# Kernel tuning notes

Hardware: AMD Instinct MI355X
Metric: run time of the kernel (lower is better)

## Reference

```python
import jax, jax.numpy as jnp
import numpy as np

B, G = 256, 24
N = B * G
D_IN, HEADS, D_HEAD = 128, 8, 64  # out_channels = in_channels//2 = 64, concat=False
EFF = HEADS * D_HEAD
EPS = 1e-5
SCALE = float(np.sqrt(D_HEAD))

def _gelu(x):
    return jax.nn.gelu(x, approximate=False)

def _pff(x, w1, b1, w2, b2):
    # PositionwiseFeedForward, dropout=0 (eval)
    return _gelu(x @ w1.T + b1) @ w2.T + b2

def _graph_norm_global(x, w, b, ms):
    # GraphNorm called without batch -> single graph over all N nodes
    mean = jnp.mean(x, axis=0, keepdims=True)
    out = x - mean * ms
    var = jnp.mean(out * out, axis=0, keepdims=True)
    return w * out / jnp.sqrt(var + EPS) + b

def _graph_norm(x, w, b, ms, batch, nseg):
    cnt = jax.ops.segment_sum(jnp.ones((x.shape[0],), x.dtype), batch, nseg)[:, None]
    mean = jax.ops.segment_sum(x, batch, nseg) / cnt
    out = x - mean[batch] * ms
    var = jax.ops.segment_sum(out * out, batch, nseg) / cnt
    return w * out / jnp.sqrt(var + EPS)[batch] + b

def _segment_softmax(logits, seg, nseg):
    m = jax.ops.segment_max(logits, seg, num_segments=nseg)
    e = jnp.exp(logits - m[seg])
    s = jax.ops.segment_sum(e, seg, num_segments=nseg)
    return e / (s[seg] + 1e-16)

def _attn_conv(x, edge_index, p):
    (nq_w, nq_b, nq_ms, wq, bq, wk, bk, wv, bv,
     no_w, no_b, no_ms, o_w1, o_b1, o_w2, o_b2) = p
    n = x.shape[0]
    xin = x
    xn = _graph_norm_global(x, nq_w, nq_b, nq_ms)
    q = (xn @ wq.T + bq).reshape(n, HEADS, D_HEAD)
    k = (xn @ wk.T + bk).reshape(n, HEADS, D_HEAD)
    v = (xn @ wv.T + bv).reshape(n, HEADS, D_HEAD)
    loops = jnp.arange(n, dtype=edge_index.dtype)  # add_self_loops appends
    src = jnp.concatenate([edge_index[0], loops])
    dst = jnp.concatenate([edge_index[1], loops])
    qk = jnp.sum(q[dst] * k[src], axis=-1) / SCALE          # [E', H]
    alpha = _segment_softmax(qk, dst, n)                     # segment softmax over dst
    aggr = jax.ops.segment_sum(v[src] * alpha[:, :, None], dst, num_segments=n)  # [N,H,Dh]
    aggr = aggr.mean(axis=1)                                 # concat=False: head mean -> [N,64]
    init = xin.reshape(n, D_IN // D_HEAD, D_HEAD).sum(axis=1)  # sum-fold 128 -> 64 residual
    h = aggr + init
    hn = _graph_norm_global(h, no_w, no_b, no_ms)
    return h + _pff(hn, o_w1, o_b1, o_w2, o_b2)


def setup_inputs() -> dict:
    key = jax.random.key(0)
    ks = jax.random.split(key, 12)
    # block-dense edges: fully connected within each set, no self loops
    a = np.arange(G)
    ii, jj = np.meshgrid(a, a, indexing='ij')
    m = ii != jj
    dst_l, src_l = ii[m], jj[m]
    offs = (np.arange(B) * G)[:, None]
    src = (src_l[None, :] + offs).reshape(-1)
    dst = (dst_l[None, :] + offs).reshape(-1)
    edge_index = jnp.asarray(np.stack([src, dst]), dtype=jnp.int64)
    batch = jnp.asarray(np.repeat(np.arange(B), G), dtype=jnp.int64)
    ptr = jnp.asarray(np.arange(B + 1) * G, dtype=jnp.int64)
    x = jax.random.normal(ks[0], (N, D_IN), jnp.float32)
    def lin(k, o, i):
        return jax.random.normal(k, (o, i), jnp.float32) * (1.0 / np.sqrt(i))
    d = dict(x=x, edge_index=edge_index, ptr=ptr, batch=batch)
    d.update(nq_w=jnp.ones((D_IN,)), nq_b=jnp.zeros((D_IN,)), nq_ms=jnp.ones((D_IN,)))
    d.update(wq=lin(ks[1], EFF, D_IN), bq=jnp.zeros((EFF,)),
             wk=lin(ks[2], EFF, D_IN), bk=jnp.zeros((EFF,)),
             wv=lin(ks[3], EFF, D_IN), bv=jnp.zeros((EFF,)))
    d.update(no_w=jnp.ones((D_HEAD,)), no_b=jnp.zeros((D_HEAD,)), no_ms=jnp.ones((D_HEAD,)))
    d.update(o_w1=lin(ks[4], D_HEAD, D_HEAD), o_b1=jnp.zeros((D_HEAD,)),
             o_w2=lin(ks[5], D_HEAD, D_HEAD), o_b2=jnp.zeros((D_HEAD,)))
    d.update(pn_w=jnp.ones((D_HEAD,)), pn_b=jnp.zeros((D_HEAD,)), pn_ms=jnp.ones((D_HEAD,)))
    d.update(p_w1=lin(ks[6], D_HEAD, D_HEAD), p_b1=jnp.zeros((D_HEAD,)),
             p_w2=lin(ks[7], 1, D_HEAD), p_b2=jnp.zeros((1,)))
    return d


def reference(x, edge_index, ptr, batch,
              nq_w, nq_b, nq_ms, wq, bq, wk, bk, wv, bv,
              no_w, no_b, no_ms, o_w1, o_b1, o_w2, o_b2,
              pn_w, pn_b, pn_ms, p_w1, p_b1, p_w2, p_b2):
    nseg = ptr.shape[0] - 1
    h = _attn_conv(x, edge_index,
                   (nq_w, nq_b, nq_ms, wq, bq, wk, bk, wv, bv,
                    no_w, no_b, no_ms, o_w1, o_b1, o_w2, o_b2))   # [N,64]
    hn = _graph_norm(h, pn_w, pn_b, pn_ms, batch, nseg)
    score = _pff(hn, p_w1, p_b1, p_w2, p_b2)                       # [N,1]
    w = _segment_softmax(score[:, 0], batch, nseg)[:, None]        # per-set softmax
    return jax.ops.segment_sum(x * w, batch, num_segments=nseg)    # [B, 128]
```

## Files before the change

kernel.cpp:

```cpp
#include <hip/hip_runtime.h>
#include <stdint.h>


#define N_NODES 6144
#define GSIZE 24
#define NGRAPH 256
#define DIN 128
#define DH 64
#define EFF 512
#define EPSN 1e-5f

typedef __attribute__((ext_vector_type(8))) __bf16 bf16x8;
typedef __attribute__((ext_vector_type(4))) float f32x4;
union U16B { uint4 u; bf16x8 v; unsigned short s[8]; };

__device__ inline unsigned short f2bf(float f){
  unsigned u = __float_as_uint(f);
  u += 0x7fff + ((u>>16)&1);
  return (unsigned short)(u>>16);
}
__device__ inline float gelu_exact(float x){ return 0.5f*x*(1.0f+erff(x*0.70710678118654752f)); }

#define XP    0
#define HP    49152
#define WT1   81920
#define WT2   86016
#define PWT1  90112
#define FBo   94208
#define WCVT_BYTE  385024
#define HCOMB_BYTE 778240

#define QSTRIDE 516

__global__ __launch_bounds__(256)
void k_pre(const float* __restrict__ x,
           const float* __restrict__ o_w1, const float* __restrict__ o_w2,
           const float* __restrict__ p_w1,
           const float* __restrict__ o_b1, const float* __restrict__ o_b2,
           const float* __restrict__ p_b1, const float* __restrict__ p_w2,
           const float* __restrict__ p_b2,
           const float* __restrict__ wq, const float* __restrict__ wk,
           const float* __restrict__ wv,
           float* __restrict__ wsf){
  int t = threadIdx.x;
  int bi = blockIdx.x;
  if(bi < 192){
    int c = t & 127, h = t >> 7;
    float s = 0.f, q = 0.f;
    #pragma unroll
    for(int r = 0; r < 16; ++r){
      float v = x[(size_t)(bi*32 + h + 2*r)*DIN + c];
      s += v; q += v*v;
    }
    __shared__ float sm[256], sm2[256];
    sm[t] = s; sm2[t] = q;
    __syncthreads();
    if(t < 128){
      wsf[XP + bi*256 + t]       = sm[t] + sm[t+128];
      wsf[XP + bi*256 + 128 + t] = sm2[t] + sm2[t+128];
    }
    return;
  }
  if(bi < 195){
    const float* src; float* dst;
    if(bi == 192){ src = o_w1; dst = wsf + WT1; }
    else if(bi == 193){ src = o_w2; dst = wsf + WT2; }
    else { src = p_w1; dst = wsf + PWT1; }
    for(int p = t; p < DH*DH; p += 256){
      int r = p >> 6, c = p & 63;
      dst[c*DH + r] = src[p];
    }
    if(bi == 192){
      float* fb = wsf + FBo;
      if(t < 64){
        fb[t]       = o_b1[t];
        fb[64 + t]  = o_b2[t];
        fb[128 + t] = p_b1[t];
        fb[192 + t] = p_w2[t];
      }
      if(t == 0) fb[256] = p_b2[0];
    }
    return;
  }
  int j = bi - 195;
  int mat = j >> 2, seg = j & 3;
  const float* src = (mat==0) ? wq : (mat==1) ? wk : wv;
  unsigned short* dst = (unsigned short*)((char*)wsf + WCVT_BYTE)
                        + (size_t)mat*EFF*DIN + seg*16384;
  const float* sp = src + seg*16384;
  for(int e = t*8; e < 16384; e += 2048){
    float4 a = *(const float4*)(sp + e);
    float4 b = *(const float4*)(sp + e + 4);
    U16B o;
    o.s[0]=f2bf(a.x); o.s[1]=f2bf(a.y); o.s[2]=f2bf(a.z); o.s[3]=f2bf(a.w);
    o.s[4]=f2bf(b.x); o.s[5]=f2bf(b.y); o.s[6]=f2bf(b.z); o.s[7]=f2bf(b.w);
    *(uint4*)(dst + e) = o.u;
  }
}

__global__ __launch_bounds__(512)
void k_attn2(const float* __restrict__ x,
             const float* __restrict__ bq, const float* __restrict__ bk,
             const float* __restrict__ bv,
             const float* __restrict__ nq_w, const float* __restrict__ nq_b,
             const float* __restrict__ nq_ms,
             float* __restrict__ ws, float* __restrict__ hcomb){
  __shared__ __align__(16) float qlds[3*GSIZE*QSTRIDE];
  __shared__ __align__(16) float hv[GSIZE][68];
  __shared__ float A1s[DIN], C1s[DIN];

  int t = threadIdx.x, g = blockIdx.x, base = g*GSIZE;
  int h = t >> 6, l = t & 63;
  const unsigned short* wcvt = (const unsigned short*)((const char*)ws + WCVT_BYTE);

  for(int i = t; i < GSIZE*68; i += 512) ((float*)hv)[i] = 0.f;

  {
    float* redA = qlds;
    float* redB = qlds + 512;
    int c = t & 127, grp = t >> 7;
    float s = 0.f, q = 0.f;
    for(int p = grp*48; p < grp*48 + 48; ++p){
      s += ws[XP + p*256 + c];
      q += ws[XP + p*256 + 128 + c];
    }
    redA[t] = s; redB[t] = q;
    __syncthreads();
    if(t < 128){
      float s1 = redA[t] + redA[t+128] + redA[t+256] + redA[t+384];
      float q1 = redB[t] + redB[t+128] + redB[t+256] + redB[t+384];
      float mean = s1 * (1.0f / N_NODES);
      float ex2  = q1 * (1.0f / N_NODES);
      float cm   = mean * nq_ms[t];
      float var  = ex2 - 2.f*cm*mean + cm*cm;
      float rstd = rsqrtf(var + EPSN);
      float a    = nq_w[t] * rstd;
      A1s[t] = a; C1s[t] = nq_b[t] - a*cm;
    }
    __syncthreads();
  }

  int m = l & 15, lq = l >> 4;

  bf16x8 afr[2][4];
  #pragma unroll
  for(int mt = 0; mt < 2; ++mt){
    int row = mt*16 + m; if(row > GSIZE-1) row = GSIZE-1;
    const float* xr = x + (size_t)(base + row)*DIN;
    #pragma unroll
    for(int kk = 0; kk < 4; ++kk){
      int k0 = kk*32 + lq*8;
      float4 a = *(const float4*)(xr + k0);
      float4 b = *(const float4*)(xr + k0 + 4);
      U16B u;
      u.s[0] = f2bf(a.x*A1s[k0+0] + C1s[k0+0]);
      u.s[1] = f2bf(a.y*A1s[k0+1] + C1s[k0+1]);
      u.s[2] = f2bf(a.z*A1s[k0+2] + C1s[k0+2]);
      u.s[3] = f2bf(a.w*A1s[k0+3] + C1s[k0+3]);
      u.s[4] = f2bf(b.x*A1s[k0+4] + C1s[k0+4]);
      u.s[5] = f2bf(b.y*A1s[k0+5] + C1s[k0+5]);
      u.s[6] = f2bf(b.z*A1s[k0+6] + C1s[k0+6]);
      u.s[7] = f2bf(b.w*A1s[k0+7] + C1s[k0+7]);
      afr[mt][kk] = u.v;
    }
  }

  #pragma unroll
  for(int nt = 0; nt < 12; ++nt){
    int mat = nt >> 2, sub = nt & 3;
    const unsigned short* wp = wcvt + (size_t)mat*EFF*DIN
                             + (size_t)(h*64 + sub*16 + m)*DIN + lq*8;
    const float* bias = (mat==0) ? bq : (mat==1) ? bk : bv;
    float4 bb = *(const float4*)(bias + h*64 + sub*16 + lq*4);
    f32x4 acc0 = {0.f,0.f,0.f,0.f}, acc1 = {0.f,0.f,0.f,0.f};
    #pragma unroll
    for(int kk = 0; kk < 4; ++kk){
      U16B w8; w8.u = *(const uint4*)(wp + kk*32);
      acc0 = __builtin_amdgcn_mfma_f32_16x16x32_bf16(w8.v, afr[0][kk], acc0, 0, 0, 0);
      acc1 = __builtin_amdgcn_mfma_f32_16x16x32_bf16(w8.v, afr[1][kk], acc1, 0, 0, 0);
    }
    float* dst = qlds + mat*(GSIZE*QSTRIDE);
    int col = h*64 + sub*16 + lq*4;
    {
      float4 o; o.x = acc0[0]+bb.x; o.y = acc0[1]+bb.y; o.z = acc0[2]+bb.z; o.w = acc0[3]+bb.w;
      *(float4*)(dst + m*QSTRIDE + col) = o;
    }
    if(m < 8){
      float4 o; o.x = acc1[0]+bb.x; o.y = acc1[1]+bb.y; o.z = acc1[2]+bb.z; o.w = acc1[3]+bb.w;
      *(float4*)(dst + (16+m)*QSTRIDE + col) = o;
    }
  }

  {
    int r0 = 3*(l >> 3), j0 = 3*(l & 7);
    const float* qp = qlds + r0*QSTRIDE + h*64;
    const float* kp = qlds + GSIZE*QSTRIDE + j0*QSTRIDE + h*64;
    float s00=0.f,s01=0.f,s02=0.f,s10=0.f,s11=0.f,s12=0.f,s20=0.f,s21=0.f,s22=0.f;
    #pragma unroll
    for(int d4 = 0; d4 < 16; ++d4){
      float4 q0 = *(const float4*)(qp + d4*4);
      float4 q1 = *(const float4*)(qp + QSTRIDE + d4*4);
      float4 q2 = *(const float4*)(qp + 2*QSTRIDE + d4*4);
      float4 k0 = *(const float4*)(kp + d4*4);
      float4 k1 = *(const float4*)(kp + QSTRIDE + d4*4);
      float4 k2 = *(const float4*)(kp + 2*QSTRIDE + d4*4);
      s00 += q0.x*k0.x + q0.y*k0.y + q0.z*k0.z + q0.w*k0.w;
      s01 += q0.x*k1.x + q0.y*k1.y + q0.z*k1.z + q0.w*k1.w;
      s02 += q0.x*k2.x + q0.y*k2.y + q0.z*k2.z + q0.w*k2.w;
      s10 += q1.x*k0.x + q1.y*k0.y + q1.z*k0.z + q1.w*k0.w;
      s11 += q1.x*k1.x + q1.y*k1.y + q1.z*k1.z + q1.w*k1.w;
      s12 += q1.x*k2.x + q1.y*k2.y + q1.z*k2.z + q1.w*k2.w;
      s20 += q2.x*k0.x + q2.y*k0.y + q2.z*k0.z + q2.w*k0.w;
      s21 += q2.x*k1.x + q2.y*k1.y + q2.z*k1.z + q2.w*k1.w;
      s22 += q2.x*k2.x + q2.y*k2.y + q2.z*k2.z + q2.w*k2.w;
    }
    float a0, a1, a2, m0, su, inv;
    float* STb = qlds + h*64;
    a0 = s00*0.125f; a1 = s01*0.125f; a2 = s02*0.125f;
    m0 = fmaxf(fmaxf(a0, a1), a2);
    #pragma unroll
    for(int o = 1; o < 8; o <<= 1) m0 = fmaxf(m0, __shfl_xor(m0, o, 8));
    a0 = __expf(a0-m0); a1 = __expf(a1-m0); a2 = __expf(a2-m0);
    su = a0 + a1 + a2;
    #pragma unroll
    for(int o = 1; o < 8; o <<= 1) su += __shfl_xor(su, o, 8);
    inv = 1.0f/(su + 1e-16f);
    STb[(j0+0)*QSTRIDE + r0] = a0*inv; STb[(j0+1)*QSTRIDE + r0] = a1*inv; STb[(j0+2)*QSTRIDE + r0] = a2*inv;
    a0 = s10*0.125f; a1 = s11*0.125f; a2 = s12*0.125f;
    m0 = fmaxf(fmaxf(a0, a1), a2);
    #pragma unroll
    for(int o = 1; o < 8; o <<= 1) m0 = fmaxf(m0, __shfl_xor(m0, o, 8));
    a0 = __expf(a0-m0); a1 = __expf(a1-m0); a2 = __expf(a2-m0);
    su = a0 + a1 + a2;
    #pragma unroll
    for(int o = 1; o < 8; o <<= 1) su += __shfl_xor(su, o, 8);
    inv = 1.0f/(su + 1e-16f);
    STb[(j0+0)*QSTRIDE + r0+1] = a0*inv; STb[(j0+1)*QSTRIDE + r0+1] = a1*inv; STb[(j0+2)*QSTRIDE + r0+1] = a2*inv;
    a0 = s20*0.125f; a1 = s21*0.125f; a2 = s22*0.125f;
    m0 = fmaxf(fmaxf(a0, a1), a2);
    #pragma unroll
    for(int o = 1; o < 8; o <<= 1) m0 = fmaxf(m0, __shfl_xor(m0, o, 8));
    a0 = __expf(a0-m0); a1 = __expf(a1-m0); a2 = __expf(a2-m0);
    su = a0 + a1 + a2;
    #pragma unroll
    for(int o = 1; o < 8; o <<= 1) su += __shfl_xor(su, o, 8);
    inv = 1.0f/(su + 1e-16f);
    STb[(j0+0)*QSTRIDE + r0+2] = a0*inv; STb[(j0+1)*QSTRIDE + r0+2] = a1*inv; STb[(j0+2)*QSTRIDE + r0+2] = a2*inv;
  }

  {
    float o24[GSIZE];
    #pragma unroll
    for(int r = 0; r < GSIZE; ++r) o24[r] = 0.f;
    const float* vp  = qlds + 2*GSIZE*QSTRIDE + h*64 + l;
    const float* STb = qlds + h*64;
    #pragma unroll
    for(int j = 0; j < GSIZE; ++j){
      float v = vp[j*QSTRIDE];
      #pragma unroll
      for(int rq = 0; rq < 6; ++rq){
        float4 p4 = *(const float4*)(STb + j*QSTRIDE + rq*4);
        o24[rq*4+0] = fmaf(p4.x, v, o24[rq*4+0]);
        o24[rq*4+1] = fmaf(p4.y, v, o24[rq*4+1]);
        o24[rq*4+2] = fmaf(p4.z, v, o24[rq*4+2]);
        o24[rq*4+3] = fmaf(p4.w, v, o24[rq*4+3]);
      }
    }
    #pragma unroll
    for(int r = 0; r < GSIZE; ++r) atomicAdd(&hv[r][l], o24[r]);
  }
  __syncthreads();

  #pragma unroll
  for(int sl = 0; sl < 3; ++sl){
    int idx = t + sl*512;
    int r = idx >> 6, d = idx & 63;
    const float* xr = x + (size_t)(base + r)*DIN;
    float hval = hv[r][d]*0.125f + xr[d] + xr[64 + d];
    hcomb[(size_t)(base + r)*DH + d] = hval;
    hv[r][d] = hval;
  }
  __syncthreads();
  if(t < 64){
    float s1 = 0.f, s2 = 0.f;
    #pragma unroll
    for(int i = 0; i < GSIZE; ++i){ float v = hv[i][t]; s1 += v; s2 += v*v; }
    ws[HP + g*128 + t]      = s1;
    ws[HP + g*128 + 64 + t] = s2;
  }
}

__global__ __launch_bounds__(256)
void k_final(const float* __restrict__ x,
             const float* __restrict__ hbuf, const float* __restrict__ ws,
             const float* __restrict__ no_w, const float* __restrict__ no_b,
             const float* __restrict__ no_ms,
             const float* __restrict__ pn_w, const float* __restrict__ pn_b,
             const float* __restrict__ pn_ms,
             float* __restrict__ out){
  __shared__ __align__(16) float W1[4096];
  __shared__ __align__(16) float W2[4096];
  __shared__ __align__(16) float PW1[4096];
  __shared__ __align__(16) float fbs[260];
  __shared__ __align__(16) float hs[GSIZE][68];
  __shared__ __align__(16) float hn[GSIZE][68];
  __shared__ __align__(16) float ts[GSIZE][68];
  __shared__ float A2s[DH], C2s[DH];
  __shared__ float a3[DH], c3[DH];
  __shared__ float scores[GSIZE], wsm[GSIZE];
  __shared__ float redA[256], redB[256];

  int t = threadIdx.x;
  int base = blockIdx.x * GSIZE;
  int c = t & 63, i0 = t >> 6;

  {
    const float4* s1 = (const float4*)(ws + WT1);
    const float4* s2 = (const float4*)(ws + WT2);
    const float4* s3 = (const float4*)(ws + PWT1);
    #pragma unroll
    for(int it = 0; it < 4; ++it){
      int i = t + it*256;
      ((float4*)W1)[i]  = s1[i];
      ((float4*)W2)[i]  = s2[i];
      ((float4*)PW1)[i] = s3[i];
    }
    if(t < 257) fbs[t] = ws[FBo + t];
    int cc = t & 63, grp = t >> 6;
    float s1r = 0.f, s2r = 0.f;
    for(int p = grp; p < NGRAPH; p += 4){
      s1r += ws[HP + p*128 + cc];
      s2r += ws[HP + p*128 + 64 + cc];
    }
    redA[t] = s1r; redB[t] = s2r;
  }
  __syncthreads();
  if(t < DH){
    float a1 = redA[t] + redA[t+64] + redA[t+128] + redA[t+192];
    float a2 = redB[t] + redB[t+64] + redB[t+128] + redB[t+192];
    float mean = a1 * (1.0f / N_NODES);
    float ex2  = a2 * (1.0f / N_NODES);
    float cm   = mean * no_ms[t];
    float var  = ex2 - 2.f*cm*mean + cm*cm;
    float rstd = rsqrtf(var + EPSN);
    float a    = no_w[t] * rstd;
    A2s[t] = a; C2s[t] = no_b[t] - a*cm;
  }
  __syncthreads();
  {
    float a2 = A2s[c];
    float c2 = C2s[c];
    #pragma unroll
    for(int r = 0; r < 6; ++r){
      int i = i0 + 4*r;
      float hvv = hbuf[(size_t)(base + i)*DH + c];
      hs[i][c] = hvv;
      hn[i][c] = a2*hvv + c2;
    }
  }
  __syncthreads();

  {
    float acc[6];
    #pragma unroll
    for(int r = 0; r < 6; ++r) acc[r] = fbs[c];
    #pragma unroll 16
    for(int k = 0; k < DH; ++k){
      float w = W1[k*DH + c];
      #pragma unroll
      for(int r = 0; r < 6; ++r) acc[r] = fmaf(hn[i0 + 4*r][k], w, acc[r]);
    }
    #pragma unroll
    for(int r = 0; r < 6; ++r) ts[i0 + 4*r][c] = gelu_exact(acc[r]);
  }
  __syncthreads();

  {
    float acc[6];
    #pragma unroll
    for(int r = 0; r < 6; ++r) acc[r] = fbs[64 + c];
    #pragma unroll 16
    for(int k = 0; k < DH; ++k){
      float w = W2[k*DH + c];
      #pragma unroll
      for(int r = 0; r < 6; ++r) acc[r] = fmaf(ts[i0 + 4*r][k], w, acc[r]);
    }
    #pragma unroll
    for(int r = 0; r < 6; ++r) hs[i0 + 4*r][c] += acc[r];
  }
  __syncthreads();

  if(t < DH){
    float s1 = 0.f, s2 = 0.f;
    #pragma unroll
    for(int i = 0; i < GSIZE; i++){ float v = hs[i][t]; s1 += v; s2 += v*v; }
    float mean = s1 * (1.0f / GSIZE);
    float ex2  = s2 * (1.0f / GSIZE);
    float cm   = mean * pn_ms[t];
    float var  = ex2 - 2.f*cm*mean + cm*cm;
    float rstd = rsqrtf(var + EPSN);
    float a    = pn_w[t] * rstd;
    a3[t] = a; c3[t] = pn_b[t] - a*cm;
  }
  __syncthreads();

  {
    float acc[6];
    #pragma unroll
    for(int r = 0; r < 6; ++r) acc[r] = fbs[128 + c];
    #pragma unroll 16
    for(int k = 0; k < DH; ++k){
      float w  = PW1[k*DH + c];
      float ak = a3[k], ck = c3[k];
      #pragma unroll
      for(int r = 0; r < 6; ++r){
        float hnv = fmaf(ak, hs[i0 + 4*r][k], ck);
        acc[r] = fmaf(hnv, w, acc[r]);
      }
    }
    #pragma unroll
    for(int r = 0; r < 6; ++r) ts[i0 + 4*r][c] = gelu_exact(acc[r]);
  }
  __syncthreads();

  if(t < GSIZE){
    const float4* tp = (const float4*)ts[t];
    const float4* wp = (const float4*)(fbs + 192);
    float s = fbs[256];
    #pragma unroll
    for(int q = 0; q < 16; ++q){
      float4 a = tp[q], b = wp[q];
      s += a.x*b.x + a.y*b.y + a.z*b.z + a.w*b.w;
    }
    scores[t] = s;
  }
  __syncthreads();
  if(t < GSIZE){
    float mx = -1e30f;
    #pragma unroll
    for(int j = 0; j < GSIZE; j++) mx = fmaxf(mx, scores[j]);
    float sum = 0.f;
    #pragma unroll
    for(int j = 0; j < GSIZE; j++) sum += __expf(scores[j] - mx);
    wsm[t] = __expf(scores[t] - mx) / (sum + 1e-16f);
  }
  __syncthreads();
  if(t < DIN){
    float s = 0.f;
    #pragma unroll 8
    for(int i = 0; i < GSIZE; i++) s += wsm[i] * x[(size_t)(base+i)*DIN + t];
    out[(size_t)blockIdx.x*DIN + t] = s;
  }
}

extern "C" void kernel_launch(void* const* d_in, const int* in_sizes, int n_in,
                              void* d_out, int out_size, void* d_ws, size_t ws_size,
                              hipStream_t stream){
  (void)in_sizes; (void)n_in; (void)out_size; (void)ws_size;
  const float* x    = (const float*)d_in[0];
  const float* nq_w = (const float*)d_in[4];
  const float* nq_b = (const float*)d_in[5];
  const float* nq_ms= (const float*)d_in[6];
  const float* wq   = (const float*)d_in[7];
  const float* bq   = (const float*)d_in[8];
  const float* wk   = (const float*)d_in[9];
  const float* bk   = (const float*)d_in[10];
  const float* wv   = (const float*)d_in[11];
  const float* bv   = (const float*)d_in[12];
  const float* no_w = (const float*)d_in[13];
  const float* no_b = (const float*)d_in[14];
  const float* no_ms= (const float*)d_in[15];
  const float* o_w1 = (const float*)d_in[16];
  const float* o_b1 = (const float*)d_in[17];
  const float* o_w2 = (const float*)d_in[18];
  const float* o_b2 = (const float*)d_in[19];
  const float* pn_w = (const float*)d_in[20];
  const float* pn_b = (const float*)d_in[21];
  const float* pn_ms= (const float*)d_in[22];
  const float* p_w1 = (const float*)d_in[23];
  const float* p_b1 = (const float*)d_in[24];
  const float* p_w2 = (const float*)d_in[25];
  const float* p_b2 = (const float*)d_in[26];

  float* ws    = (float*)d_ws;
  float* hcomb = (float*)((char*)d_ws + HCOMB_BYTE);

  k_pre<<<207, 256, 0, stream>>>(x, o_w1, o_w2, p_w1, o_b1, o_b2, p_b1, p_w2, p_b2,
                                 wq, wk, wv, ws);
  k_attn2<<<NGRAPH, 512, 0, stream>>>(x, bq, bk, bv, nq_w, nq_b, nq_ms, ws, hcomb);
  k_final<<<NGRAPH, 256, 0, stream>>>(x, hcomb, ws, no_w, no_b, no_ms,
                                      pn_w, pn_b, pn_ms, (float*)d_out);
}
```

Baseline: 181.0 us.

## Reduce global norm statistics with atomics and software-pipeline QKV weight loads

The per-block column sums and sums of squares for both global GraphNorms are now accumulated with atomicAdd into small buffers that are zeroed by a memset. Each consumer block reads one finished value instead of re-reducing 192 or 256 partials, which removes redundant reduction work in every block of k_attn2 and k_final. The QKV MFMA loop is also unrolled by hand with triple-buffered weight registers so global loads overlap the MFMAs. The costs are an extra memset launch, atomic contention, nondeterministic float summation order, and higher register pressure.

```diff
diff --git a/kernel.cpp b/kernel.cpp
--- a/kernel.cpp
+++ b/kernel.cpp
@@ -21,8 +21,8 @@
 }
 __device__ inline float gelu_exact(float x){ return 0.5f*x*(1.0f+erff(x*0.70710678118654752f)); }
 
-#define XP    0
-#define HP    49152
+#define XS    0
+#define HS    256
 #define WT1   81920
 #define WT2   86016
 #define PWT1  90112
@@ -56,8 +56,8 @@
     sm[t] = s; sm2[t] = q;
     __syncthreads();
     if(t < 128){
-      wsf[XP + bi*256 + t]       = sm[t] + sm[t+128];
-      wsf[XP + bi*256 + 128 + t] = sm2[t] + sm2[t+128];
+      atomicAdd(&wsf[XS + t],       sm[t] + sm[t+128]);
+      atomicAdd(&wsf[XS + 128 + t], sm2[t] + sm2[t+128]);
     }
     return;
   }
@@ -98,6 +98,40 @@
   }
 }
 
+#define LOADW(nt, W, B) do{ \
+  const int mat_ = (nt)>>2, sub_ = (nt)&3; \
+  const unsigned short* wp_ = wcvt + (size_t)mat_*EFF*DIN \
+      + (size_t)(h*64 + sub_*16 + m)*DIN + lq*8; \
+  W[0] = *(const uint4*)(wp_);      W[1] = *(const uint4*)(wp_ + 32); \
+  W[2] = *(const uint4*)(wp_ + 64); W[3] = *(const uint4*)(wp_ + 96); \
+  const float* bias_ = (mat_==0) ? bq : (mat_==1) ? bk : bv; \
+  B = *(const float4*)(bias_ + h*64 + sub_*16 + lq*4); \
+}while(0)
+
+#define COMPW(nt, W, B) do{ \
+  const int mat_ = (nt)>>2, sub_ = (nt)&3; \
+  f32x4 a0_ = {0.f,0.f,0.f,0.f}, a1_ = {0.f,0.f,0.f,0.f}; \
+  U16B w8_; \
+  w8_.u = W[0]; \
+  a0_ = __builtin_amdgcn_mfma_f32_16x16x32_bf16(w8_.v, afr[0][0], a0_, 0, 0, 0); \
+  a1_ = __builtin_amdgcn_mfma_f32_16x16x32_bf16(w8_.v, afr[1][0], a1_, 0, 0, 0); \
+  w8_.u = W[1]; \
+  a0_ = __builtin_amdgcn_mfma_f32_16x16x32_bf16(w8_.v, afr[0][1], a0_, 0, 0, 0); \
+  a1_ = __builtin_amdgcn_mfma_f32_16x16x32_bf16(w8_.v, afr[1][1], a1_, 0, 0, 0); \
+  w8_.u = W[2]; \
+  a0_ = __builtin_amdgcn_mfma_f32_16x16x32_bf16(w8_.v, afr[0][2], a0_, 0, 0, 0); \
+  a1_ = __builtin_amdgcn_mfma_f32_16x16x32_bf16(w8_.v, afr[1][2], a1_, 0, 0, 0); \
+  w8_.u = W[3]; \
+  a0_ = __builtin_amdgcn_mfma_f32_16x16x32_bf16(w8_.v, afr[0][3], a0_, 0, 0, 0); \
+  a1_ = __builtin_amdgcn_mfma_f32_16x16x32_bf16(w8_.v, afr[1][3], a1_, 0, 0, 0); \
+  float* dst_ = qlds + mat_*(GSIZE*QSTRIDE); \
+  const int col_ = h*64 + sub_*16 + lq*4; \
+  { float4 o_; o_.x=a0_[0]+B.x; o_.y=a0_[1]+B.y; o_.z=a0_[2]+B.z; o_.w=a0_[3]+B.w; \
+    *(float4*)(dst_ + m*QSTRIDE + col_) = o_; } \
+  if(m < 8){ float4 o_; o_.x=a1_[0]+B.x; o_.y=a1_[1]+B.y; o_.z=a1_[2]+B.z; o_.w=a1_[3]+B.w; \
+    *(float4*)(dst_ + (16+m)*QSTRIDE + col_) = o_; } \
+}while(0)
+
 __global__ __launch_bounds__(512)
 void k_attn2(const float* __restrict__ x,
              const float* __restrict__ bq, const float* __restrict__ bk,
@@ -115,30 +149,18 @@
 
   for(int i = t; i < GSIZE*68; i += 512) ((float*)hv)[i] = 0.f;
 
-  {
-    float* redA = qlds;
-    float* redB = qlds + 512;
-    int c = t & 127, grp = t >> 7;
-    float s = 0.f, q = 0.f;
-    for(int p = grp*48; p < grp*48 + 48; ++p){
-      s += ws[XP + p*256 + c];
-      q += ws[XP + p*256 + 128 + c];
-    }
-    redA[t] = s; redB[t] = q;
-    __syncthreads();
-    if(t < 128){
-      float s1 = redA[t] + redA[t+128] + redA[t+256] + redA[t+384];
-      float q1 = redB[t] + redB[t+128] + redB[t+256] + redB[t+384];
-      float mean = s1 * (1.0f / N_NODES);
-      float ex2  = q1 * (1.0f / N_NODES);
-      float cm   = mean * nq_ms[t];
-      float var  = ex2 - 2.f*cm*mean + cm*cm;
-      float rstd = rsqrtf(var + EPSN);
-      float a    = nq_w[t] * rstd;
-      A1s[t] = a; C1s[t] = nq_b[t] - a*cm;
-    }
-    __syncthreads();
-  }
+  if(t < 128){
+    float s1 = ws[XS + t];
+    float q1 = ws[XS + 128 + t];
+    float mean = s1 * (1.0f / N_NODES);
+    float ex2  = q1 * (1.0f / N_NODES);
+    float cm   = mean * nq_ms[t];
+    float var  = ex2 - 2.f*cm*mean + cm*cm;
+    float rstd = rsqrtf(var + EPSN);
+    float a    = nq_w[t] * rstd;
+    A1s[t] = a; C1s[t] = nq_b[t] - a*cm;
+  }
+  __syncthreads();
 
   int m = l & 15, lq = l >> 4;
 
@@ -165,30 +187,22 @@
     }
   }
 
-  #pragma unroll
-  for(int nt = 0; nt < 12; ++nt){
-    int mat = nt >> 2, sub = nt & 3;
-    const unsigned short* wp = wcvt + (size_t)mat*EFF*DIN
-                             + (size_t)(h*64 + sub*16 + m)*DIN + lq*8;
-    const float* bias = (mat==0) ? bq : (mat==1) ? bk : bv;
-    float4 bb = *(const float4*)(bias + h*64 + sub*16 + lq*4);
-    f32x4 acc0 = {0.f,0.f,0.f,0.f}, acc1 = {0.f,0.f,0.f,0.f};
-    #pragma unroll
-    for(int kk = 0; kk < 4; ++kk){
-      U16B w8; w8.u = *(const uint4*)(wp + kk*32);
-      acc0 = __builtin_amdgcn_mfma_f32_16x16x32_bf16(w8.v, afr[0][kk], acc0, 0, 0, 0);
-      acc1 = __builtin_amdgcn_mfma_f32_16x16x32_bf16(w8.v, afr[1][kk], acc1, 0, 0, 0);
-    }
-    float* dst = qlds + mat*(GSIZE*QSTRIDE);
-    int col = h*64 + sub*16 + lq*4;
-    {
-      float4 o; o.x = acc0[0]+bb.x; o.y = acc0[1]+bb.y; o.z = acc0[2]+bb.z; o.w = acc0[3]+bb.w;
-      *(float4*)(dst + m*QSTRIDE + col) = o;
-    }
-    if(m < 8){
-      float4 o; o.x = acc1[0]+bb.x; o.y = acc1[1]+bb.y; o.z = acc1[2]+bb.z; o.w = acc1[3]+bb.w;
-      *(float4*)(dst + (16+m)*QSTRIDE + col) = o;
-    }
+  {
+    uint4 wA[4], wB[4], wC[4];
+    float4 bA, bB, bC;
+    LOADW(0, wA, bA);  LOADW(1, wB, bB);
+    LOADW(2, wC, bC);  COMPW(0, wA, bA);
+    LOADW(3, wA, bA);  COMPW(1, wB, bB);
+    LOADW(4, wB, bB);  COMPW(2, wC, bC);
+    LOADW(5, wC, bC);  COMPW(3, wA, bA);
+    LOADW(6, wA, bA);  COMPW(4, wB, bB);
+    LOADW(7, wB, bB);  COMPW(5, wC, bC);
+    LOADW(8, wC, bC);  COMPW(6, wA, bA);
+    LOADW(9, wA, bA);  COMPW(7, wB, bB);
+    LOADW(10, wB, bB); COMPW(8, wC, bC);
+    LOADW(11, wC, bC); COMPW(9, wA, bA);
+    COMPW(10, wB, bB);
+    COMPW(11, wC, bC);
   }
 
   {
@@ -285,8 +299,8 @@
     float s1 = 0.f, s2 = 0.f;
     #pragma unroll
     for(int i = 0; i < GSIZE; ++i){ float v = hv[i][t]; s1 += v; s2 += v*v; }
-    ws[HP + g*128 + t]      = s1;
-    ws[HP + g*128 + 64 + t] = s2;
+    atomicAdd(&ws[HS + t],      s1);
+    atomicAdd(&ws[HS + 64 + t], s2);
   }
 }
 
@@ -308,7 +322,6 @@
   __shared__ float A2s[DH], C2s[DH];
   __shared__ float a3[DH], c3[DH];
   __shared__ float scores[GSIZE], wsm[GSIZE];
-  __shared__ float redA[256], redB[256];
 
   int t = threadIdx.x;
   int base = blockIdx.x * GSIZE;
@@ -326,25 +339,17 @@
       ((float4*)PW1)[i] = s3[i];
     }
     if(t < 257) fbs[t] = ws[FBo + t];
-    int cc = t & 63, grp = t >> 6;
-    float s1r = 0.f, s2r = 0.f;
-    for(int p = grp; p < NGRAPH; p += 4){
-      s1r += ws[HP + p*128 + cc];
-      s2r += ws[HP + p*128 + 64 + cc];
-    }
-    redA[t] = s1r; redB[t] = s2r;
-  }
-  __syncthreads();
-  if(t < DH){
-    float a1 = redA[t] + redA[t+64] + redA[t+128] + redA[t+192];
-    float a2 = redB[t] + redB[t+64] + redB[t+128] + redB[t+192];
-    float mean = a1 * (1.0f / N_NODES);
-    float ex2  = a2 * (1.0f / N_NODES);
-    float cm   = mean * no_ms[t];
-    float var  = ex2 - 2.f*cm*mean + cm*cm;
-    float rstd = rsqrtf(var + EPSN);
-    float a    = no_w[t] * rstd;
-    A2s[t] = a; C2s[t] = no_b[t] - a*cm;
+    if(t < DH){
+      float a1 = ws[HS + t];
+      float a2 = ws[HS + 64 + t];
+      float mean = a1 * (1.0f / N_NODES);
+      float ex2  = a2 * (1.0f / N_NODES);
+      float cm   = mean * no_ms[t];
+      float var  = ex2 - 2.f*cm*mean + cm*cm;
+      float rstd = rsqrtf(var + EPSN);
+      float a    = no_w[t] * rstd;
+      A2s[t] = a; C2s[t] = no_b[t] - a*cm;
+    }
   }
   __syncthreads();
   {
@@ -485,6 +490,7 @@
   float* ws    = (float*)d_ws;
   float* hcomb = (float*)((char*)d_ws + HCOMB_BYTE);
 
+  hipMemsetAsync(d_ws, 0, 384*sizeof(float), stream);
   k_pre<<<207, 256, 0, stream>>>(x, o_w1, o_w2, p_w1, o_b1, o_b2, p_b1, p_w2, p_b2,
                                  wq, wk, wv, ws);
   k_attn2<<<NGRAPH, 512, 0, stream>>>(x, bq, bk, bv, nq_w, nq_b, nq_ms, ws, hcomb);
```

New measurement: 171.2 us. 5.4% less time.
